# Kernel tuning notes

Measured on AMD Instinct MI355X. Metric: run time of the kernel, lower is better.

The kernel has to match this reference:

```python
import jax, jax.numpy as jnp
import numpy as np
from jax import lax

B, C_IN, L = 16, 4, 300000
KERNEL, ANCHOR_N = 11, 16
LEAK = 1e-4
EPS = 1e-12  # torch F.normalize eps


def setup_inputs() -> dict:
    key = jax.random.key(0)
    k1, k2, k3 = jax.random.split(key, 3)
    data = jax.random.normal(k1, (B, C_IN, L), dtype=jnp.float32)
    # Conv1d weights, PyTorch default init scale ~ U(-s, s), s = 1/sqrt(fan_in)
    s = 1.0 / np.sqrt(C_IN * KERNEL)
    W = jax.random.uniform(k2, (ANCHOR_N, C_IN, KERNEL), dtype=jnp.float32, minval=-s, maxval=s)
    b = jax.random.uniform(k3, (ANCHOR_N,), dtype=jnp.float32, minval=-s, maxval=s)
    return {"data": data, "W": W, "b": b, "anchor_index": 3}


def reference(data, W, b, anchor_index):
    # Conv1d(4 -> anchor_n, valid padding) + LeakyReLU(0.0001)
    y = lax.conv_general_dilated(
        data, W, window_strides=(1,), padding="VALID",
        dimension_numbers=("NCH", "OIH", "NCH"))
    y = y + b[None, :, None]                      # [B, anchor_n, Lc]
    y = jnp.where(y > 0, y, LEAK * y)
    # select anchor channel, add leading dim -> [1, B, Lc]
    ch = y[:, anchor_index, :][None]
    # F.normalize(dim=2, p=1)
    denom = jnp.maximum(jnp.sum(jnp.abs(ch), axis=2, keepdims=True), EPS)
    channel = ch / denom
    # softmax over sequence dim (gamma = 1)
    dist = jax.nn.softmax(channel, axis=2)
    # weighted moments of position distribution (single pass each)
    Lc = dist.shape[2]
    x = jnp.arange(Lc, dtype=dist.dtype)          # positions
    mean = jnp.sum(dist * x, axis=2, keepdims=True)    # [1,B,1]
    x_diff = x - mean                                   # [1,B,Lc]
    var = jnp.sum(dist * x_diff * x_diff, axis=2, keepdims=True)
    z = x_diff / jnp.sqrt(var)
    z3 = z * z * z
    skews = jnp.mean(z3, axis=2)                  # [1,B]
    kts = jnp.mean(z3 * z, axis=2) - 3.0          # [1,B]
    return (skews, kts, channel)
```

## Files before the change

kernel.cpp:

```cpp
#include <hip/hip_runtime.h>
#include <math.h>

#define BATCH 16
#define CIN 4
#define LEN 300000
#define KW 11
#define LC (LEN - KW + 1)
#define LCP 300000
#define LEAK 1e-4f
#define EPS_N 1e-12f

#define TPB 256
#define EPT 4
#define ITER 4
#define BPB (TPB * EPT * ITER)
#define NBX ((LC + BPB - 1) / BPB)


__global__ __launch_bounds__(256) void conv_stats(
    const float* __restrict__ data, const float* __restrict__ W,
    const float* __restrict__ bias, const int* __restrict__ aidx,
    float* __restrict__ ch, double* __restrict__ absP, float* __restrict__ maxP)
{
    const int b = blockIdx.y, j = blockIdx.x, tid = threadIdx.x;
    const int a = aidx[0];

    float w[CIN * KW];
#pragma unroll
    for (int k = 0; k < CIN * KW; ++k) w[k] = W[a * CIN * KW + k];
    const float sb = bias[a];

    const float* dbase = data + (size_t)b * (CIN * (size_t)LEN);
    float* chrow = ch + (size_t)b * LCP;
    const int o0 = j * BPB + tid * EPT;

    float aabs = 0.0f, amax = -INFINITY;

#pragma unroll
    for (int it = 0; it < ITER; ++it) {
        const int o = o0 + it * (TPB * EPT);
        if (o <= LC - EPT && o + 16 <= LEN) {
            float acc0 = sb, acc1 = sb, acc2 = sb, acc3 = sb;
#pragma unroll
            for (int c = 0; c < CIN; ++c) {
                const float* src = dbase + (size_t)c * LEN + o;
                const float4 v0 = *(const float4*)(src);
                const float4 v1 = *(const float4*)(src + 4);
                const float4 v2 = *(const float4*)(src + 8);
                const float4 v3 = *(const float4*)(src + 12);
                float x[16] = { v0.x, v0.y, v0.z, v0.w,  v1.x, v1.y, v1.z, v1.w,
                                v2.x, v2.y, v2.z, v2.w,  v3.x, v3.y, v3.z, v3.w };
#pragma unroll
                for (int k = 0; k < KW; ++k) {
                    const float wv = w[c * KW + k];
                    acc0 = fmaf(x[k],     wv, acc0);
                    acc1 = fmaf(x[k + 1], wv, acc1);
                    acc2 = fmaf(x[k + 2], wv, acc2);
                    acc3 = fmaf(x[k + 3], wv, acc3);
                }
            }
            float4 y;
            y.x = acc0 > 0.0f ? acc0 : LEAK * acc0;
            y.y = acc1 > 0.0f ? acc1 : LEAK * acc1;
            y.z = acc2 > 0.0f ? acc2 : LEAK * acc2;
            y.w = acc3 > 0.0f ? acc3 : LEAK * acc3;
            *(float4*)(chrow + o) = y;
            aabs += (fabsf(y.x) + fabsf(y.y)) + (fabsf(y.z) + fabsf(y.w));
            amax = fmaxf(amax, fmaxf(fmaxf(y.x, y.y), fmaxf(y.z, y.w)));
        } else {
            for (int l = o; l < min(o + EPT, LC); ++l) {
                float accv = sb;
#pragma unroll
                for (int c = 0; c < CIN; ++c)
#pragma unroll
                    for (int k = 0; k < KW; ++k)
                        accv = fmaf(dbase[(size_t)c * LEN + l + k], w[c * KW + k], accv);
                const float y = accv > 0.0f ? accv : LEAK * accv;
                chrow[l] = y;
                aabs += fabsf(y);
                amax = fmaxf(amax, y);
            }
        }
    }

#pragma unroll
    for (int off = 32; off; off >>= 1) {
        aabs += __shfl_down(aabs, off);
        amax = fmaxf(amax, __shfl_down(amax, off));
    }
    __shared__ float ra[4], rm[4];
    const int wv = tid >> 6;
    if ((tid & 63) == 0) { ra[wv] = aabs; rm[wv] = amax; }
    __syncthreads();
    if (tid == 0) {
        absP[b * NBX + j] = (double)((ra[0] + ra[1]) + (ra[2] + ra[3]));
        maxP[b * NBX + j] = fmaxf(fmaxf(rm[0], rm[1]), fmaxf(rm[2], rm[3]));
    }
}

__global__ __launch_bounds__(256) void softmax_pass(
    const float* __restrict__ ch, const double* __restrict__ absP,
    const float* __restrict__ maxP, float* __restrict__ chan_out,
    double* __restrict__ sP)
{
    const int b = blockIdx.y, j = blockIdx.x, tid = threadIdx.x;

    __shared__ float sstat[2];
    if (tid < 64) {
        double s = 0.0; float m = -INFINITY;
        for (int i = tid; i < NBX; i += 64) {
            s += absP[b * NBX + i];
            m = fmaxf(m, maxP[b * NBX + i]);
        }
#pragma unroll
        for (int off = 32; off; off >>= 1) {
            s += __shfl_down(s, off);
            m = fmaxf(m, __shfl_down(m, off));
        }
        if (tid == 0) {
            sstat[0] = fmaxf((float)s, EPS_N);
            sstat[1] = m;
        }
    }
    __syncthreads();
    const float inv = 1.0f / sstat[0];
    const float mx  = sstat[1] * inv;

    const float* src = ch + (size_t)b * LCP;
    float* dst = chan_out + (size_t)b * LC;
    const int o0 = j * BPB + tid * EPT;

    double te = 0.0, t1 = 0.0, t2 = 0.0;

#pragma unroll
    for (int it = 0; it < ITER; ++it) {
        const int o = o0 + it * (TPB * EPT);
        if (o <= LC - EPT) {
            const float4 v = *(const float4*)(src + o);
            const float c0 = v.x * inv, c1 = v.y * inv, c2 = v.z * inv, c3 = v.w * inv;
            if ((b & 1) == 0) {
                *(float4*)(dst + o) = make_float4(c0, c1, c2, c3);
            } else {
                *(float2*)(dst + o)     = make_float2(c0, c1);
                *(float2*)(dst + o + 2) = make_float2(c2, c3);
            }
            const float e0 = expf(c0 - mx), e1 = expf(c1 - mx);
            const float e2 = expf(c2 - mx), e3 = expf(c3 - mx);
            const float se  = (e0 + e1) + (e2 + e3);
            const float su  = e1 + 2.0f * e2 + 3.0f * e3;
            const float suu = e1 + 4.0f * e2 + 9.0f * e3;
            const double od = (double)o;
            te += (double)se;
            t1 += od * (double)se + (double)su;
            t2 += od * od * (double)se + 2.0 * od * (double)su + (double)suu;
        } else {
            for (int l = o; l < LC; ++l) {
                const float c = src[l] * inv;
                dst[l] = c;
                const float e = expf(c - mx);
                const double xd = (double)l;
                te += (double)e;
                t1 += (double)e * xd;
                t2 += (double)e * xd * xd;
            }
        }
    }

#pragma unroll
    for (int off = 32; off; off >>= 1) {
        te += __shfl_down(te, off);
        t1 += __shfl_down(t1, off);
        t2 += __shfl_down(t2, off);
    }
    __shared__ double we[4], w1[4], w2[4];
    const int wv = tid >> 6;
    if ((tid & 63) == 0) { we[wv] = te; w1[wv] = t1; w2[wv] = t2; }
    __syncthreads();
    if (tid == 0) {
        double* p = sP + (size_t)(b * NBX + j) * 3;
        p[0] = (we[0] + we[1]) + (we[2] + we[3]);
        p[1] = (w1[0] + w1[1]) + (w1[2] + w1[3]);
        p[2] = (w2[0] + w2[1]) + (w2[2] + w2[3]);
    }
}

__global__ void finalize(const double* __restrict__ sP, float* __restrict__ out)
{
    const int b = blockIdx.x, t = threadIdx.x;
    double te = 0.0, t1 = 0.0, t2 = 0.0;
    for (int i = t; i < NBX; i += 64) {
        const double* p = sP + (size_t)(b * NBX + i) * 3;
        te += p[0]; t1 += p[1]; t2 += p[2];
    }
#pragma unroll
    for (int off = 32; off; off >>= 1) {
        te += __shfl_down(te, off);
        t1 += __shfl_down(t1, off);
        t2 += __shfl_down(t2, off);
    }
    if (t == 0) {
        const double E    = te;
        const double mean = t1 / E;
        const double var  = t2 / E - mean * mean;

        const double n   = (double)LC;
        const double nm1 = n - 1.0;
        const double S1p = 0.5 * n * nm1;
        const double S2p = nm1 * n * (2.0 * n - 1.0) / 6.0;
        const double S3p = S1p * S1p;
        const double S4p = S2p * (3.0 * n * n - 3.0 * n - 1.0) / 5.0;

        const double mu  = mean;
        const double mu2 = mu * mu;
        const double P3 = S3p - 3.0 * mu * S2p + 3.0 * mu2 * S1p - n * mu * mu2;
        const double P4 = S4p - 4.0 * mu * S3p + 6.0 * mu2 * S2p
                          - 4.0 * mu * mu2 * S1p + n * mu2 * mu2;

        const double sv = sqrt(var);
        out[b]         = (float)(P3 / (n * sv * sv * sv));
        out[BATCH + b] = (float)(P4 / (n * var * var) - 3.0);
    }
}

extern "C" void kernel_launch(void* const* d_in, const int* in_sizes, int n_in,
                              void* d_out, int out_size, void* d_ws, size_t ws_size,
                              hipStream_t stream) {
    const float* data = (const float*)d_in[0];
    const float* W    = (const float*)d_in[1];
    const float* bias = (const float*)d_in[2];
    const int*   aidx = (const int*)d_in[3];
    float* out = (float*)d_out;

    char* ws = (char*)d_ws;
    double* absP = (double*)(ws + 0);
    float*  maxP = (float*) (ws + 16384);
    double* sP   = (double*)(ws + 32768);
    float*  ch   = (float*) (ws + 131072);

    dim3 grid(NBX, BATCH);
    conv_stats<<<grid, dim3(TPB), 0, stream>>>(data, W, bias, aidx, ch, absP, maxP);
    softmax_pass<<<grid, dim3(TPB), 0, stream>>>(ch, absP, maxP, out + 2 * BATCH, sP);
    finalize<<<dim3(BATCH), dim3(64), 0, stream>>>(sP, out);
}
```

Measured before the change: 135.8 us.

## Fuse conv, softmax and finalize into one cooperative kernel with grid syncs

Replaces the three-kernel pipeline with a single cooperative kernel of 64x16 blocks that keeps conv outputs in registers across two grid-wide syncs. The intermediate channel buffer is no longer written to and re-read from global memory, and two launches go away. The change costs grid.sync overhead, more registers per thread (20 floats of outputs are held), and fixed chunk sizes. A fallback three-kernel path runs if occupancy is too low for all blocks to be resident.

Result: faster. 133.1 us (-2.0%).

```diff
diff --git a/kernel.cpp b/kernel.cpp
--- a/kernel.cpp
+++ b/kernel.cpp
@@ -1,5 +1,8 @@
 #include <hip/hip_runtime.h>
+#include <hip/hip_cooperative_groups.h>
 #include <math.h>
+
+namespace cg = cooperative_groups;
 
 #define BATCH 16
 #define CIN 4
@@ -12,16 +15,84 @@
 
 #define TPB 256
 #define EPT 4
-#define ITER 4
-#define BPB (TPB * EPT * ITER)
-#define NBX ((LC + BPB - 1) / BPB)
-
-
-__global__ __launch_bounds__(256) void conv_stats(
+#define NBX 64
+#define NBLK (NBX * BATCH)
+#define CHUNK 4688
+#define ITER 5
+
+
+__device__ inline void conv_iter_fast(const float* __restrict__ src,
+                                      const float* w, float sb, float* yo)
+{
+    float acc0 = sb, acc1 = sb, acc2 = sb, acc3 = sb;
+#pragma unroll
+    for (int c = 0; c < CIN; ++c) {
+        const float* s = src + (size_t)c * LEN;
+        const float4 v0 = *(const float4*)(s);
+        const float4 v1 = *(const float4*)(s + 4);
+        const float4 v2 = *(const float4*)(s + 8);
+        const float4 v3 = *(const float4*)(s + 12);
+        float x[16] = { v0.x, v0.y, v0.z, v0.w,  v1.x, v1.y, v1.z, v1.w,
+                        v2.x, v2.y, v2.z, v2.w,  v3.x, v3.y, v3.z, v3.w };
+#pragma unroll
+        for (int k = 0; k < KW; ++k) {
+            const float wv = w[c * KW + k];
+            acc0 = fmaf(x[k],     wv, acc0);
+            acc1 = fmaf(x[k + 1], wv, acc1);
+            acc2 = fmaf(x[k + 2], wv, acc2);
+            acc3 = fmaf(x[k + 3], wv, acc3);
+        }
+    }
+    yo[0] = acc0 > 0.0f ? acc0 : LEAK * acc0;
+    yo[1] = acc1 > 0.0f ? acc1 : LEAK * acc1;
+    yo[2] = acc2 > 0.0f ? acc2 : LEAK * acc2;
+    yo[3] = acc3 > 0.0f ? acc3 : LEAK * acc3;
+}
+
+__device__ inline float conv_one(const float* __restrict__ dbase, int l,
+                                 const float* w, float sb)
+{
+    float acc = sb;
+#pragma unroll
+    for (int c = 0; c < CIN; ++c)
+#pragma unroll
+        for (int k = 0; k < KW; ++k)
+            acc = fmaf(dbase[(size_t)c * LEN + l + k], w[c * KW + k], acc);
+    return acc > 0.0f ? acc : LEAK * acc;
+}
+
+__device__ inline void finalize_row(double e, double m1, double m2,
+                                    float* __restrict__ out, int b)
+{
+    const double mean = m1 / e;
+    const double var  = m2 / e - mean * mean;
+
+    const double n   = (double)LC;
+    const double nm1 = n - 1.0;
+    const double S1p = 0.5 * n * nm1;
+    const double S2p = nm1 * n * (2.0 * n - 1.0) / 6.0;
+    const double S3p = S1p * S1p;
+    const double S4p = S2p * (3.0 * n * n - 3.0 * n - 1.0) / 5.0;
+
+    const double mu  = mean;
+    const double mu2 = mu * mu;
+    const double P3 = S3p - 3.0 * mu * S2p + 3.0 * mu2 * S1p - n * mu * mu2;
+    const double P4 = S4p - 4.0 * mu * S3p + 6.0 * mu2 * S2p
+                      - 4.0 * mu * mu2 * S1p + n * mu2 * mu2;
+
+    const double sv = sqrt(var);
+    out[b]         = (float)(P3 / (n * sv * sv * sv));
+    out[BATCH + b] = (float)(P4 / (n * var * var) - 3.0);
+}
+
+__global__ __launch_bounds__(256, 4) void fused(
     const float* __restrict__ data, const float* __restrict__ W,
     const float* __restrict__ bias, const int* __restrict__ aidx,
-    float* __restrict__ ch, double* __restrict__ absP, float* __restrict__ maxP)
-{
+    float* __restrict__ out,
+    double* __restrict__ absP, float* __restrict__ maxP, double* __restrict__ sP)
+{
+    cg::grid_group grid = cg::this_grid();
+
     const int b = blockIdx.y, j = blockIdx.x, tid = threadIdx.x;
     const int a = aidx[0];
 
@@ -31,54 +102,31 @@
     const float sb = bias[a];
 
     const float* dbase = data + (size_t)b * (CIN * (size_t)LEN);
-    float* chrow = ch + (size_t)b * LCP;
-    const int o0 = j * BPB + tid * EPT;
-
+    const int cstart = j * CHUNK;
+    const int cend   = min(cstart + CHUNK, LC);
+
+    float y[ITER][EPT];
     float aabs = 0.0f, amax = -INFINITY;
 
 #pragma unroll
     for (int it = 0; it < ITER; ++it) {
-        const int o = o0 + it * (TPB * EPT);
-        if (o <= LC - EPT && o + 16 <= LEN) {
-            float acc0 = sb, acc1 = sb, acc2 = sb, acc3 = sb;
-#pragma unroll
-            for (int c = 0; c < CIN; ++c) {
-                const float* src = dbase + (size_t)c * LEN + o;
-                const float4 v0 = *(const float4*)(src);
-                const float4 v1 = *(const float4*)(src + 4);
-                const float4 v2 = *(const float4*)(src + 8);
-                const float4 v3 = *(const float4*)(src + 12);
-                float x[16] = { v0.x, v0.y, v0.z, v0.w,  v1.x, v1.y, v1.z, v1.w,
-                                v2.x, v2.y, v2.z, v2.w,  v3.x, v3.y, v3.z, v3.w };
-#pragma unroll
-                for (int k = 0; k < KW; ++k) {
-                    const float wv = w[c * KW + k];
-                    acc0 = fmaf(x[k],     wv, acc0);
-                    acc1 = fmaf(x[k + 1], wv, acc1);
-                    acc2 = fmaf(x[k + 2], wv, acc2);
-                    acc3 = fmaf(x[k + 3], wv, acc3);
+        const int o = cstart + it * (TPB * EPT) + tid * EPT;
+        if (o + EPT <= cend && o + 16 <= LEN) {
+            conv_iter_fast(dbase + o, w, sb, y[it]);
+            aabs += (fabsf(y[it][0]) + fabsf(y[it][1])) +
+                    (fabsf(y[it][2]) + fabsf(y[it][3]));
+            amax = fmaxf(amax, fmaxf(fmaxf(y[it][0], y[it][1]),
+                                     fmaxf(y[it][2], y[it][3])));
+        } else {
+#pragma unroll
+            for (int u = 0; u < EPT; ++u) {
+                const int l = o + u;
+                if (l < cend) {
+                    const float v = conv_one(dbase, l, w, sb);
+                    y[it][u] = v;
+                    aabs += fabsf(v);
+                    amax = fmaxf(amax, v);
                 }
-            }
-            float4 y;
-            y.x = acc0 > 0.0f ? acc0 : LEAK * acc0;
-            y.y = acc1 > 0.0f ? acc1 : LEAK * acc1;
-            y.z = acc2 > 0.0f ? acc2 : LEAK * acc2;
-            y.w = acc3 > 0.0f ? acc3 : LEAK * acc3;
-            *(float4*)(chrow + o) = y;
-            aabs += (fabsf(y.x) + fabsf(y.y)) + (fabsf(y.z) + fabsf(y.w));
-            amax = fmaxf(amax, fmaxf(fmaxf(y.x, y.y), fmaxf(y.z, y.w)));
-        } else {
-            for (int l = o; l < min(o + EPT, LC); ++l) {
-                float accv = sb;
-#pragma unroll
-                for (int c = 0; c < CIN; ++c)
-#pragma unroll
-                    for (int k = 0; k < KW; ++k)
-                        accv = fmaf(dbase[(size_t)c * LEN + l + k], w[c * KW + k], accv);
-                const float y = accv > 0.0f ? accv : LEAK * accv;
-                chrow[l] = y;
-                aabs += fabsf(y);
-                amax = fmaxf(amax, y);
             }
         }
     }
@@ -96,22 +144,13 @@
         absP[b * NBX + j] = (double)((ra[0] + ra[1]) + (ra[2] + ra[3]));
         maxP[b * NBX + j] = fmaxf(fmaxf(rm[0], rm[1]), fmaxf(rm[2], rm[3]));
     }
-}
-
-__global__ __launch_bounds__(256) void softmax_pass(
-    const float* __restrict__ ch, const double* __restrict__ absP,
-    const float* __restrict__ maxP, float* __restrict__ chan_out,
-    double* __restrict__ sP)
-{
-    const int b = blockIdx.y, j = blockIdx.x, tid = threadIdx.x;
+
+    grid.sync();
 
     __shared__ float sstat[2];
     if (tid < 64) {
-        double s = 0.0; float m = -INFINITY;
-        for (int i = tid; i < NBX; i += 64) {
-            s += absP[b * NBX + i];
-            m = fmaxf(m, maxP[b * NBX + i]);
-        }
+        double s = absP[b * NBX + tid];
+        float  m = maxP[b * NBX + tid];
 #pragma unroll
         for (int off = 32; off; off >>= 1) {
             s += __shfl_down(s, off);
@@ -126,18 +165,16 @@
     const float inv = 1.0f / sstat[0];
     const float mx  = sstat[1] * inv;
 
-    const float* src = ch + (size_t)b * LCP;
-    float* dst = chan_out + (size_t)b * LC;
-    const int o0 = j * BPB + tid * EPT;
+    float* dst = out + 2 * BATCH + (size_t)b * LC;
 
     double te = 0.0, t1 = 0.0, t2 = 0.0;
 
 #pragma unroll
     for (int it = 0; it < ITER; ++it) {
-        const int o = o0 + it * (TPB * EPT);
-        if (o <= LC - EPT) {
-            const float4 v = *(const float4*)(src + o);
-            const float c0 = v.x * inv, c1 = v.y * inv, c2 = v.z * inv, c3 = v.w * inv;
+        const int o = cstart + it * (TPB * EPT) + tid * EPT;
+        if (o + EPT <= cend && o + 16 <= LEN) {
+            const float c0 = y[it][0] * inv, c1 = y[it][1] * inv;
+            const float c2 = y[it][2] * inv, c3 = y[it][3] * inv;
             if ((b & 1) == 0) {
                 *(float4*)(dst + o) = make_float4(c0, c1, c2, c3);
             } else {
@@ -154,7 +191,156 @@
             t1 += od * (double)se + (double)su;
             t2 += od * od * (double)se + 2.0 * od * (double)su + (double)suu;
         } else {
-            for (int l = o; l < LC; ++l) {
+#pragma unroll
+            for (int u = 0; u < EPT; ++u) {
+                const int l = o + u;
+                if (l < cend) {
+                    const float c = y[it][u] * inv;
+                    dst[l] = c;
+                    const float e = expf(c - mx);
+                    const double xd = (double)l;
+                    te += (double)e;
+                    t1 += (double)e * xd;
+                    t2 += (double)e * xd * xd;
+                }
+            }
+        }
+    }
+
+#pragma unroll
+    for (int off = 32; off; off >>= 1) {
+        te += __shfl_down(te, off);
+        t1 += __shfl_down(t1, off);
+        t2 += __shfl_down(t2, off);
+    }
+    __shared__ double we[4], w1[4], w2[4];
+    if ((tid & 63) == 0) { we[wv] = te; w1[wv] = t1; w2[wv] = t2; }
+    __syncthreads();
+    if (tid == 0) {
+        double* p = sP + (size_t)(b * NBX + j) * 3;
+        p[0] = (we[0] + we[1]) + (we[2] + we[3]);
+        p[1] = (w1[0] + w1[1]) + (w1[2] + w1[3]);
+        p[2] = (w2[0] + w2[1]) + (w2[2] + w2[3]);
+    }
+
+    grid.sync();
+
+    if (j == 0 && tid < 64) {
+        const double* p = sP + (size_t)(b * NBX + tid) * 3;
+        double e = p[0], m1 = p[1], m2 = p[2];
+#pragma unroll
+        for (int off = 32; off; off >>= 1) {
+            e  += __shfl_down(e, off);
+            m1 += __shfl_down(m1, off);
+            m2 += __shfl_down(m2, off);
+        }
+        if (tid == 0) finalize_row(e, m1, m2, out, b);
+    }
+}
+
+__global__ __launch_bounds__(256) void conv_stats_fb(
+    const float* __restrict__ data, const float* __restrict__ W,
+    const float* __restrict__ bias, const int* __restrict__ aidx,
+    float* __restrict__ ch, double* __restrict__ absP, float* __restrict__ maxP)
+{
+    const int b = blockIdx.y, j = blockIdx.x, tid = threadIdx.x;
+    const int a = aidx[0];
+    float w[CIN * KW];
+#pragma unroll
+    for (int k = 0; k < CIN * KW; ++k) w[k] = W[a * CIN * KW + k];
+    const float sb = bias[a];
+
+    const float* dbase = data + (size_t)b * (CIN * (size_t)LEN);
+    float* chrow = ch + (size_t)b * LCP;
+    const int cstart = j * CHUNK;
+    const int cend   = min(cstart + CHUNK, LC);
+
+    float aabs = 0.0f, amax = -INFINITY;
+#pragma unroll
+    for (int it = 0; it < ITER; ++it) {
+        const int o = cstart + it * (TPB * EPT) + tid * EPT;
+        if (o + EPT <= cend && o + 16 <= LEN) {
+            float yv[EPT];
+            conv_iter_fast(dbase + o, w, sb, yv);
+            *(float4*)(chrow + o) = make_float4(yv[0], yv[1], yv[2], yv[3]);
+            aabs += (fabsf(yv[0]) + fabsf(yv[1])) + (fabsf(yv[2]) + fabsf(yv[3]));
+            amax = fmaxf(amax, fmaxf(fmaxf(yv[0], yv[1]), fmaxf(yv[2], yv[3])));
+        } else {
+            for (int l = o; l < min(o + EPT, cend); ++l) {
+                const float v = conv_one(dbase, l, w, sb);
+                chrow[l] = v;
+                aabs += fabsf(v);
+                amax = fmaxf(amax, v);
+            }
+        }
+    }
+
+#pragma unroll
+    for (int off = 32; off; off >>= 1) {
+        aabs += __shfl_down(aabs, off);
+        amax = fmaxf(amax, __shfl_down(amax, off));
+    }
+    __shared__ float ra[4], rm[4];
+    const int wv = tid >> 6;
+    if ((tid & 63) == 0) { ra[wv] = aabs; rm[wv] = amax; }
+    __syncthreads();
+    if (tid == 0) {
+        absP[b * NBX + j] = (double)((ra[0] + ra[1]) + (ra[2] + ra[3]));
+        maxP[b * NBX + j] = fmaxf(fmaxf(rm[0], rm[1]), fmaxf(rm[2], rm[3]));
+    }
+}
+
+__global__ __launch_bounds__(256) void softmax_fb(
+    const float* __restrict__ ch, const double* __restrict__ absP,
+    const float* __restrict__ maxP, float* __restrict__ chan_out,
+    double* __restrict__ sP)
+{
+    const int b = blockIdx.y, j = blockIdx.x, tid = threadIdx.x;
+
+    __shared__ float sstat[2];
+    if (tid < 64) {
+        double s = absP[b * NBX + tid];
+        float  m = maxP[b * NBX + tid];
+#pragma unroll
+        for (int off = 32; off; off >>= 1) {
+            s += __shfl_down(s, off);
+            m = fmaxf(m, __shfl_down(m, off));
+        }
+        if (tid == 0) { sstat[0] = fmaxf((float)s, EPS_N); sstat[1] = m; }
+    }
+    __syncthreads();
+    const float inv = 1.0f / sstat[0];
+    const float mx  = sstat[1] * inv;
+
+    const float* src = ch + (size_t)b * LCP;
+    float* dst = chan_out + (size_t)b * LC;
+    const int cstart = j * CHUNK;
+    const int cend   = min(cstart + CHUNK, LC);
+
+    double te = 0.0, t1 = 0.0, t2 = 0.0;
+#pragma unroll
+    for (int it = 0; it < ITER; ++it) {
+        const int o = cstart + it * (TPB * EPT) + tid * EPT;
+        if (o + EPT <= cend) {
+            const float4 v = *(const float4*)(src + o);
+            const float c0 = v.x * inv, c1 = v.y * inv, c2 = v.z * inv, c3 = v.w * inv;
+            if ((b & 1) == 0) {
+                *(float4*)(dst + o) = make_float4(c0, c1, c2, c3);
+            } else {
+                *(float2*)(dst + o)     = make_float2(c0, c1);
+                *(float2*)(dst + o + 2) = make_float2(c2, c3);
+            }
+            const float e0 = expf(c0 - mx), e1 = expf(c1 - mx);
+            const float e2 = expf(c2 - mx), e3 = expf(c3 - mx);
+            const float se  = (e0 + e1) + (e2 + e3);
+            const float su  = e1 + 2.0f * e2 + 3.0f * e3;
+            const float suu = e1 + 4.0f * e2 + 9.0f * e3;
+            const double od = (double)o;
+            te += (double)se;
+            t1 += od * (double)se + (double)su;
+            t2 += od * od * (double)se + 2.0 * od * (double)su + (double)suu;
+        } else {
+            for (int l = o; l < cend; ++l) {
                 const float c = src[l] * inv;
                 dst[l] = c;
                 const float e = expf(c - mx);
@@ -184,42 +370,18 @@
     }
 }
 
-__global__ void finalize(const double* __restrict__ sP, float* __restrict__ out)
+__global__ void finalize_fb(const double* __restrict__ sP, float* __restrict__ out)
 {
     const int b = blockIdx.x, t = threadIdx.x;
-    double te = 0.0, t1 = 0.0, t2 = 0.0;
-    for (int i = t; i < NBX; i += 64) {
-        const double* p = sP + (size_t)(b * NBX + i) * 3;
-        te += p[0]; t1 += p[1]; t2 += p[2];
-    }
+    const double* p = sP + (size_t)(b * NBX + t) * 3;
+    double te = p[0], t1 = p[1], t2 = p[2];
 #pragma unroll
     for (int off = 32; off; off >>= 1) {
         te += __shfl_down(te, off);
         t1 += __shfl_down(t1, off);
         t2 += __shfl_down(t2, off);
     }
-    if (t == 0) {
-        const double E    = te;
-        const double mean = t1 / E;
-        const double var  = t2 / E - mean * mean;
-
-        const double n   = (double)LC;
-        const double nm1 = n - 1.0;
-        const double S1p = 0.5 * n * nm1;
-        const double S2p = nm1 * n * (2.0 * n - 1.0) / 6.0;
-        const double S3p = S1p * S1p;
-        const double S4p = S2p * (3.0 * n * n - 3.0 * n - 1.0) / 5.0;
-
-        const double mu  = mean;
-        const double mu2 = mu * mu;
-        const double P3 = S3p - 3.0 * mu * S2p + 3.0 * mu2 * S1p - n * mu * mu2;
-        const double P4 = S4p - 4.0 * mu * S3p + 6.0 * mu2 * S2p
-                          - 4.0 * mu * mu2 * S1p + n * mu2 * mu2;
-
-        const double sv = sqrt(var);
-        out[b]         = (float)(P3 / (n * sv * sv * sv));
-        out[BATCH + b] = (float)(P4 / (n * var * var) - 3.0);
-    }
+    if (t == 0) finalize_row(te, t1, t2, out, b);
 }
 
 extern "C" void kernel_launch(void* const* d_in, const int* in_sizes, int n_in,
@@ -233,12 +395,26 @@
 
     char* ws = (char*)d_ws;
     double* absP = (double*)(ws + 0);
-    float*  maxP = (float*) (ws + 16384);
-    double* sP   = (double*)(ws + 32768);
-    float*  ch   = (float*) (ws + 131072);
-
-    dim3 grid(NBX, BATCH);
-    conv_stats<<<grid, dim3(TPB), 0, stream>>>(data, W, bias, aidx, ch, absP, maxP);
-    softmax_pass<<<grid, dim3(TPB), 0, stream>>>(ch, absP, maxP, out + 2 * BATCH, sP);
-    finalize<<<dim3(BATCH), dim3(64), 0, stream>>>(sP, out);
-}
+    float*  maxP = (float*) (ws + 8192);
+    double* sP   = (double*)(ws + 16384);
+    float*  ch   = (float*) (ws + 65536);
+
+    int bpc = 0;
+    hipError_t oe = hipOccupancyMaxActiveBlocksPerMultiprocessor(
+        &bpc, (const void*)fused, TPB, 0);
+    const bool coop_ok = (oe == hipSuccess) && (bpc * 256 >= NBLK);
+
+    if (coop_ok) {
+        void* args[] = { (void*)&data, (void*)&W, (void*)&bias, (void*)&aidx,
+                         (void*)&out, (void*)&absP, (void*)&maxP, (void*)&sP };
+        hipLaunchCooperativeKernel((const void*)fused, dim3(NBX, BATCH), dim3(TPB),
+                                   args, 0, stream);
+    } else {
+        dim3 grid(NBX, BATCH);
+        conv_stats_fb<<<grid, dim3(TPB), 0, stream>>>(data, W, bias, aidx, ch,
+                                                      absP, maxP);
+        softmax_fb<<<grid, dim3(TPB), 0, stream>>>(ch, absP, maxP,
+                                                   out + 2 * BATCH, sP);
+        finalize_fb<<<dim3(BATCH), dim3(64), 0, stream>>>(sP, out);
+    }
+}
```
